# Kernel tuning notes

Hardware: AMD Instinct MI355X
Metric: run time of the kernel (lower is better)

The kernel has to match this reference:

```python
import jax, jax.numpy as jnp
import numpy as np

RADIUS = 1.3
RES = 128
SH_DEG = 2
N_SH = (SH_DEG + 1) ** 2          # 9 SH basis functions
DATA_DIM = N_SH * 3 + 1           # 28: 27 SH rgb coeffs + 1 sigma
STEP = (2.0 * RADIUS / RES) / 2.0 # half a voxel, as in calc_step_size
N_INTRS = int(np.ceil(np.sqrt(3.0) * 2.0 * RES))  # torch.arange(float) length
N_RAYS = 4096


def sh_basis(d):
    # Real spherical harmonics up to degree 2, svox2/plenoxels convention. d: [B,3]
    x, y, z = d[:, 0], d[:, 1], d[:, 2]
    return jnp.stack([
        0.28209479177387814 * jnp.ones_like(x),
        -0.4886025119029199 * y,
        0.4886025119029199 * z,
        -0.4886025119029199 * x,
        1.0925484305920792 * x * y,
        -1.0925484305920792 * y * z,
        0.31539156525252005 * (2.0 * z * z - x * x - y * y),
        -1.0925484305920792 * x * z,
        0.5462742152960396 * (x * x - y * y),
    ], axis=-1)  # [B, 9]


def trilerp(grid, pts):
    # grid: [C, R, R, R] laid out (D,H,W); pts: [N,3] as (x,y,z) in [-1,1],
    # x indexes W, y indexes H, z indexes D (torch grid_sample convention),
    # align_corners=True, padding_mode='border'. Returns [C, N].
    R = grid.shape[-1]
    c = jnp.clip((pts + 1.0) * 0.5 * (R - 1), 0.0, R - 1)  # border padding
    c0 = jnp.floor(c)
    f = c - c0
    i0 = c0.astype(jnp.int32)
    i1 = jnp.minimum(i0 + 1, R - 1)
    x0, y0, z0 = i0[:, 0], i0[:, 1], i0[:, 2]
    x1, y1, z1 = i1[:, 0], i1[:, 1], i1[:, 2]
    fx, fy, fz = f[:, 0], f[:, 1], f[:, 2]
    g = lambda zi, yi, xi: grid[:, zi, yi, xi]  # [C, N]
    out = (g(z0, y0, x0) * ((1 - fz) * (1 - fy) * (1 - fx)) +
           g(z0, y0, x1) * ((1 - fz) * (1 - fy) * fx) +
           g(z0, y1, x0) * ((1 - fz) * fy * (1 - fx)) +
           g(z0, y1, x1) * ((1 - fz) * fy * fx) +
           g(z1, y0, x0) * (fz * (1 - fy) * (1 - fx)) +
           g(z1, y0, x1) * (fz * (1 - fy) * fx) +
           g(z1, y1, x0) * (fz * fy * (1 - fx)) +
           g(z1, y1, x1) * (fz * fy * fx))
    return out


def setup_inputs() -> dict:
    key = jax.random.key(0)
    k1, k2, k3 = jax.random.split(key, 3)
    rays_o = jax.random.normal(k1, (N_RAYS, 3), jnp.float32) * 0.3  # inside cube
    rd = jax.random.normal(k2, (N_RAYS, 3), jnp.float32)
    rays_d = rd / jnp.linalg.norm(rd, axis=-1, keepdims=True)
    # grid parameter: SH coeffs init 0.1, sigma init 0.01 (as in module) + noise
    base = jnp.concatenate([
        jnp.full((1, DATA_DIM - 1, RES, RES, RES), 0.1, jnp.float32),
        jnp.full((1, 1, RES, RES, RES), 0.01, jnp.float32)], axis=1)
    data = base + 0.01 * jax.random.normal(k3, (1, DATA_DIM, RES, RES, RES), jnp.float32)
    return {"rays_o": rays_o, "rays_d": rays_d, "data": data}


def reference(rays_o, rays_d, data):
    # --- ray/box intersection sampling (no grad in original) ---
    ro = jax.lax.stop_gradient(rays_o)
    rd = jax.lax.stop_gradient(rays_d)
    off_pos = (RADIUS - ro) / rd
    off_neg = (-RADIUS - ro) / rd
    start = jnp.max(jnp.minimum(off_pos, off_neg), axis=-1, keepdims=True)  # [B,1]
    steps = jnp.arange(N_INTRS, dtype=ro.dtype)[None, :]
    intersections = start + steps * STEP          # [B, N_INTRS]
    t = intersections[:, :-1]                     # [B, NI]
    pts = ro[:, None, :] + t[..., None] * rd[:, None, :]  # [B, NI, 3]
    mask = jnp.all((pts > -RADIUS) & (pts < RADIUS), axis=-1)  # [B, NI]
    ptsn = pts / RADIUS
    B, NI = t.shape

    # --- trilinear interpolation of grid at all sample points ---
    interp = trilerp(data[0], ptsn.reshape(-1, 3)).T  # [B*NI, 28]
    sigma = jax.nn.relu(interp[:, -1].reshape(B, NI))
    sigma = jnp.where(mask, sigma, 0.0)  # masked_scatter into zeros

    # --- sigma2alpha: standard volumetric compositing weights ---
    dists = (intersections[:, 1:] - intersections[:, :-1]) \
            * jnp.linalg.norm(rays_d, axis=-1, keepdims=True)  # [B, NI]
    alpha = 1.0 - jnp.exp(-sigma * dists)
    trans = jnp.cumprod(jnp.concatenate(
        [jnp.ones((B, 1), alpha.dtype), 1.0 - alpha + 1e-10], axis=1), axis=1)[:, :-1]
    abs_light = alpha * trans  # [B, NI]

    # --- SH -> rgb per sample ---
    sh_mult = sh_basis(rays_d)  # [B, 9]
    sh = interp[:, :-1].reshape(B, NI, 3, N_SH)
    rgb_pts = jnp.einsum('bk,bnck->bnc', sh_mult, sh)  # [B, NI, 3]
    rgb_pts = jnp.where(mask[..., None], rgb_pts, 0.0)  # masked_scatter

    # --- shrgb2rgb: sigmoid, composite, white background ---
    rgb = jnp.sum(abs_light[..., None] * jax.nn.sigmoid(rgb_pts), axis=1)  # [B,3]
    rgb = rgb + (1.0 - jnp.sum(abs_light, axis=1))[..., None]  # white bkgd
    return rgb
```

## Files before the change

kernel.cpp:

```cpp
#include <hip/hip_runtime.h>
#include <math.h>


typedef _Float16 h8 __attribute__((ext_vector_type(8)));

namespace {
constexpr float kRadius   = 1.3f;
constexpr int   kRes      = 128;
constexpr float kStep     = 2.0f * 1.3f / 128.0f / 2.0f;
constexpr int   kNI       = 443;
constexpr int   kNRays    = 4096;
constexpr int   kChStride = kRes * kRes * kRes;
constexpr int   kChunks   = 7;
constexpr int   kCh       = 28;
constexpr int   kVoxPad   = 32;
constexpr size_t kVoxBytes = (size_t)kChStride * kVoxPad * sizeof(_Float16);
}

__global__ __launch_bounds__(256)
void convert_grid(const float* __restrict__ grid, _Float16* __restrict__ vox)
{
    const int v = blockIdx.x * 256 + threadIdx.x;
    h8 o[4];
    #pragma unroll
    for (int c = 0; c < kCh; ++c)
        o[c >> 3][c & 7] = (_Float16)grid[c * kChStride + v];
    o[3][4] = o[3][5] = o[3][6] = o[3][7] = (_Float16)0.f;

    h8* dst = (h8*)(vox + (size_t)v * kVoxPad);
    dst[0] = o[0]; dst[1] = o[1]; dst[2] = o[2]; dst[3] = o[3];
}

__global__ __launch_bounds__(256)
void render_chunks(const float* __restrict__ rays_o,
                   const float* __restrict__ rays_d,
                   const _Float16* __restrict__ vox,
                   float* __restrict__ partials)
{
    const int lane  = threadIdx.x & 63;
    const int W     = blockIdx.x * 4 + (threadIdx.x >> 6);
    const int ray   = W / 7;
    const int chunk = W - ray * 7;

    const float ox = rays_o[3*ray+0], oy = rays_o[3*ray+1], oz = rays_o[3*ray+2];
    const float dx = rays_d[3*ray+0], dy = rays_d[3*ray+1], dz = rays_d[3*ray+2];

    const float sx = fminf(( kRadius - ox)/dx, (-kRadius - ox)/dx);
    const float sy = fminf(( kRadius - oy)/dy, (-kRadius - oy)/dy);
    const float sz = fminf(( kRadius - oz)/dz, (-kRadius - oz)/dz);
    const float start = fmaxf(sx, fmaxf(sy, sz));
    const float dnorm = sqrtf(dx*dx + dy*dy + dz*dz);
    const float dist  = kStep * dnorm;

    float shm[9];
    shm[0] =  0.28209479177387814f;
    shm[1] = -0.4886025119029199f * dy;
    shm[2] =  0.4886025119029199f * dz;
    shm[3] = -0.4886025119029199f * dx;
    shm[4] =  1.0925484305920792f * dx * dy;
    shm[5] = -1.0925484305920792f * dy * dz;
    shm[6] =  0.31539156525252005f * (2.0f*dz*dz - dx*dx - dy*dy);
    shm[7] = -1.0925484305920792f * dx * dz;
    shm[8] =  0.5462742152960396f * (dx*dx - dy*dy);

    const int k = chunk * 64 + lane;

    float alpha = 0.0f;
    float a     = 1.0f;
    float rp0 = 0.f, rp1 = 0.f, rp2 = 0.f;
    bool  inb = false;

    if (k < kNI) {
        const float t  = start + (float)k * kStep;
        const float px = ox + t*dx;
        const float py = oy + t*dy;
        const float pz = oz + t*dz;
        inb = (px > -kRadius) && (px < kRadius) &&
              (py > -kRadius) && (py < kRadius) &&
              (pz > -kRadius) && (pz < kRadius);

        float sig = 0.0f;
        if (inb) {
            const float cx = fminf(fmaxf((px*(1.0f/kRadius) + 1.0f)*0.5f*127.0f, 0.0f), 127.0f);
            const float cy = fminf(fmaxf((py*(1.0f/kRadius) + 1.0f)*0.5f*127.0f, 0.0f), 127.0f);
            const float cz = fminf(fmaxf((pz*(1.0f/kRadius) + 1.0f)*0.5f*127.0f, 0.0f), 127.0f);
            const float fx0 = floorf(cx), fy0 = floorf(cy), fz0 = floorf(cz);
            const float fx = cx - fx0, fy = cy - fy0, fz = cz - fz0;
            const int ix0 = (int)fx0, iy0 = (int)fy0, iz0 = (int)fz0;
            const int ix1 = min(ix0 + 1, 127);
            const int iy1 = min(iy0 + 1, 127);
            const int iz1 = min(iz0 + 1, 127);

            const float gx0 = 1.0f - fx, gy0 = 1.0f - fy, gz0 = 1.0f - fz;

            const int offs[8] = {
                iz0*(kRes*kRes) + iy0*kRes + ix0,
                iz0*(kRes*kRes) + iy0*kRes + ix1,
                iz0*(kRes*kRes) + iy1*kRes + ix0,
                iz0*(kRes*kRes) + iy1*kRes + ix1,
                iz1*(kRes*kRes) + iy0*kRes + ix0,
                iz1*(kRes*kRes) + iy0*kRes + ix1,
                iz1*(kRes*kRes) + iy1*kRes + ix0,
                iz1*(kRes*kRes) + iy1*kRes + ix1 };
            const float cw[8] = {
                gz0*gy0*gx0, gz0*gy0*fx, gz0*fy*gx0, gz0*fy*fx,
                fz *gy0*gx0, fz *gy0*fx, fz *fy*gx0, fz *fy*fx };

            #pragma unroll
            for (int cn = 0; cn < 8; ++cn) {
                const h8* vp = (const h8*)(vox + (size_t)offs[cn] * kVoxPad);
                const h8 q0 = vp[0], q1 = vp[1], q2 = vp[2], q3 = vp[3];

                float f[28];
                #pragma unroll
                for (int i = 0; i < 8; ++i) f[i]      = (float)q0[i];
                #pragma unroll
                for (int i = 0; i < 8; ++i) f[8 + i]  = (float)q1[i];
                #pragma unroll
                for (int i = 0; i < 8; ++i) f[16 + i] = (float)q2[i];
                #pragma unroll
                for (int i = 0; i < 4; ++i) f[24 + i] = (float)q3[i];

                float r = 0.f, g = 0.f, b = 0.f;
                #pragma unroll
                for (int j = 0; j < 9; ++j) {
                    r = fmaf(shm[j], f[j],      r);
                    g = fmaf(shm[j], f[9 + j],  g);
                    b = fmaf(shm[j], f[18 + j], b);
                }
                const float wc = cw[cn];
                rp0 = fmaf(wc, r, rp0);
                rp1 = fmaf(wc, g, rp1);
                rp2 = fmaf(wc, b, rp2);
                sig = fmaf(wc, f[27], sig);
            }
            sig = fmaxf(sig, 0.0f);
        }
        alpha = 1.0f - expf(-sig * dist);
        a     = 1.0f - alpha + 1e-10f;
    }

    float prod = a;
    #pragma unroll
    for (int off = 1; off < 64; off <<= 1) {
        const float y = __shfl_up(prod, off, 64);
        if (lane >= off) prod *= y;
    }
    float excl = __shfl_up(prod, 1, 64);
    if (lane == 0) excl = 1.0f;

    const float w = alpha * excl;

    float sR = 0.f, sG = 0.f, sB = 0.f;
    if (inb) {
        sR = w * (1.0f / (1.0f + expf(-rp0)));
        sG = w * (1.0f / (1.0f + expf(-rp1)));
        sB = w * (1.0f / (1.0f + expf(-rp2)));
    }
    float sL = w;

    const float P = __shfl(prod, 63, 64);

    #pragma unroll
    for (int off = 32; off > 0; off >>= 1) {
        sR += __shfl_down(sR, off, 64);
        sG += __shfl_down(sG, off, 64);
        sB += __shfl_down(sB, off, 64);
        sL += __shfl_down(sL, off, 64);
    }

    if (lane == 0) {
        float* p = partials + (size_t)(ray * 7 + chunk) * 5;
        p[0] = sR; p[1] = sG; p[2] = sB; p[3] = sL; p[4] = P;
    }
}

__global__ __launch_bounds__(256)
void combine_chunks(const float* __restrict__ partials, float* __restrict__ out)
{
    const int r = blockIdx.x * 256 + threadIdx.x;
    const float* p = partials + (size_t)r * (kChunks * 5);

    float carry = 1.0f, aR = 0.f, aG = 0.f, aB = 0.f, aL = 0.f;
    #pragma unroll
    for (int c = 0; c < kChunks; ++c) {
        aR = fmaf(carry, p[c*5 + 0], aR);
        aG = fmaf(carry, p[c*5 + 1], aG);
        aB = fmaf(carry, p[c*5 + 2], aB);
        aL = fmaf(carry, p[c*5 + 3], aL);
        carry *= p[c*5 + 4];
    }
    const float bg = 1.0f - aL;
    out[3*r + 0] = aR + bg;
    out[3*r + 1] = aG + bg;
    out[3*r + 2] = aB + bg;
}

#define TRI8(p) (w000*(p)[o000] + w001*(p)[o001] + w010*(p)[o010] + w011*(p)[o011] \
               + w100*(p)[o100] + w101*(p)[o101] + w110*(p)[o110] + w111*(p)[o111])

__global__ __launch_bounds__(256)
void plenoxel_render_direct(const float* __restrict__ rays_o,
                            const float* __restrict__ rays_d,
                            const float* __restrict__ grid,
                            float* __restrict__ out)
{
    const int lane = threadIdx.x & 63;
    const int ray  = blockIdx.x * 4 + (threadIdx.x >> 6);

    const float ox = rays_o[3*ray+0], oy = rays_o[3*ray+1], oz = rays_o[3*ray+2];
    const float dx = rays_d[3*ray+0], dy = rays_d[3*ray+1], dz = rays_d[3*ray+2];

    const float sx = fminf(( kRadius - ox)/dx, (-kRadius - ox)/dx);
    const float sy = fminf(( kRadius - oy)/dy, (-kRadius - oy)/dy);
    const float sz = fminf(( kRadius - oz)/dz, (-kRadius - oz)/dz);
    const float start = fmaxf(sx, fmaxf(sy, sz));
    const float dnorm = sqrtf(dx*dx + dy*dy + dz*dz);

    float shm[9];
    shm[0] =  0.28209479177387814f;
    shm[1] = -0.4886025119029199f * dy;
    shm[2] =  0.4886025119029199f * dz;
    shm[3] = -0.4886025119029199f * dx;
    shm[4] =  1.0925484305920792f * dx * dy;
    shm[5] = -1.0925484305920792f * dy * dz;
    shm[6] =  0.31539156525252005f * (2.0f*dz*dz - dx*dx - dy*dy);
    shm[7] = -1.0925484305920792f * dx * dz;
    shm[8] =  0.5462742152960396f * (dx*dx - dy*dy);

    float carry = 1.0f;
    float accR = 0.f, accG = 0.f, accB = 0.f, accL = 0.f;

    for (int chunk = 0; chunk < kChunks; ++chunk) {
        const int k = chunk * 64 + lane;
        float alpha = 0.0f, a = 1.0f;
        float rp0 = 0.f, rp1 = 0.f, rp2 = 0.f;
        bool inb = false;

        if (k < kNI) {
            const float t = start + (float)k * kStep;
            const float dist = kStep * dnorm;
            const float px = ox + t*dx, py = oy + t*dy, pz = oz + t*dz;
            inb = (px > -kRadius) && (px < kRadius) &&
                  (py > -kRadius) && (py < kRadius) &&
                  (pz > -kRadius) && (pz < kRadius);
            float sigma = 0.0f;
            if (inb) {
                const float cx = fminf(fmaxf((px*(1.0f/kRadius) + 1.0f)*0.5f*127.0f, 0.0f), 127.0f);
                const float cy = fminf(fmaxf((py*(1.0f/kRadius) + 1.0f)*0.5f*127.0f, 0.0f), 127.0f);
                const float cz = fminf(fmaxf((pz*(1.0f/kRadius) + 1.0f)*0.5f*127.0f, 0.0f), 127.0f);
                const float fx0 = floorf(cx), fy0 = floorf(cy), fz0 = floorf(cz);
                const float fx = cx - fx0, fy = cy - fy0, fz = cz - fz0;
                const int ix0 = (int)fx0, iy0 = (int)fy0, iz0 = (int)fz0;
                const int ix1 = min(ix0 + 1, 127);
                const int iy1 = min(iy0 + 1, 127);
                const int iz1 = min(iz0 + 1, 127);
                const float gx0 = 1.0f - fx, gy0 = 1.0f - fy, gz0 = 1.0f - fz;
                const float w000 = gz0*gy0*gx0, w001 = gz0*gy0*fx;
                const float w010 = gz0*fy *gx0, w011 = gz0*fy *fx;
                const float w100 = fz *gy0*gx0, w101 = fz *gy0*fx;
                const float w110 = fz *fy *gx0, w111 = fz *fy *fx;
                const int o000 = iz0*(kRes*kRes) + iy0*kRes + ix0;
                const int o001 = iz0*(kRes*kRes) + iy0*kRes + ix1;
                const int o010 = iz0*(kRes*kRes) + iy1*kRes + ix0;
                const int o011 = iz0*(kRes*kRes) + iy1*kRes + ix1;
                const int o100 = iz1*(kRes*kRes) + iy0*kRes + ix0;
                const int o101 = iz1*(kRes*kRes) + iy0*kRes + ix1;
                const int o110 = iz1*(kRes*kRes) + iy1*kRes + ix0;
                const int o111 = iz1*(kRes*kRes) + iy1*kRes + ix1;
                #pragma unroll
                for (int kk = 0; kk < 9; ++kk) {
                    rp0 = fmaf(shm[kk], TRI8(grid + (kk     ) * kChStride), rp0);
                    rp1 = fmaf(shm[kk], TRI8(grid + (kk +  9) * kChStride), rp1);
                    rp2 = fmaf(shm[kk], TRI8(grid + (kk + 18) * kChStride), rp2);
                }
                sigma = fmaxf(TRI8(grid + 27 * kChStride), 0.0f);
            }
            alpha = 1.0f - expf(-sigma * dist);
            a     = 1.0f - alpha + 1e-10f;
        }

        float prod = a;
        #pragma unroll
        for (int off = 1; off < 64; off <<= 1) {
            const float y = __shfl_up(prod, off, 64);
            if (lane >= off) prod *= y;
        }
        float excl = __shfl_up(prod, 1, 64);
        if (lane == 0) excl = 1.0f;
        const float trans = carry * excl;
        const float w = alpha * trans;
        if (inb) {
            accR = fmaf(w, 1.0f / (1.0f + expf(-rp0)), accR);
            accG = fmaf(w, 1.0f / (1.0f + expf(-rp1)), accG);
            accB = fmaf(w, 1.0f / (1.0f + expf(-rp2)), accB);
        }
        accL += w;
        carry *= __shfl(prod, 63, 64);
    }

    #pragma unroll
    for (int off = 32; off > 0; off >>= 1) {
        accR += __shfl_down(accR, off, 64);
        accG += __shfl_down(accG, off, 64);
        accB += __shfl_down(accB, off, 64);
        accL += __shfl_down(accL, off, 64);
    }

    if (lane == 0) {
        const float bg = 1.0f - accL;
        out[3*ray + 0] = accR + bg;
        out[3*ray + 1] = accG + bg;
        out[3*ray + 2] = accB + bg;
    }
}

extern "C" void kernel_launch(void* const* d_in, const int* in_sizes, int n_in,
                              void* d_out, int out_size, void* d_ws, size_t ws_size,
                              hipStream_t stream) {
    const float* rays_o = (const float*)d_in[0];
    const float* rays_d = (const float*)d_in[1];
    const float* data   = (const float*)d_in[2];
    float* out = (float*)d_out;

    const size_t partBytes = (size_t)kNRays * kChunks * 5 * sizeof(float);
    const size_t need = kVoxBytes + partBytes;

    if (ws_size >= need) {
        _Float16* vox = (_Float16*)d_ws;
        float* partials = (float*)((char*)d_ws + kVoxBytes);

        hipLaunchKernelGGL(convert_grid,
                           dim3(kChStride / 256), dim3(256), 0, stream,
                           data, vox);
        hipLaunchKernelGGL(render_chunks,
                           dim3(kNRays * kChunks / 4), dim3(256), 0, stream,
                           rays_o, rays_d, vox, partials);
        hipLaunchKernelGGL(combine_chunks,
                           dim3(kNRays / 256), dim3(256), 0, stream,
                           partials, out);
    } else {
        hipLaunchKernelGGL(plenoxel_render_direct,
                           dim3(kNRays / 4), dim3(256), 0, stream,
                           rays_o, rays_d, data, out);
    }
}
```

Before: 435.6 us.

## Process two 64-sample segments per wave and cut ray chunks to four

```diff
diff --git a/kernel.cpp b/kernel.cpp
--- a/kernel.cpp
+++ b/kernel.cpp
@@ -11,10 +11,11 @@
 constexpr int   kNI       = 443;
 constexpr int   kNRays    = 4096;
 constexpr int   kChStride = kRes * kRes * kRes;
-constexpr int   kChunks   = 7;
 constexpr int   kCh       = 28;
 constexpr int   kVoxPad   = 32;
 constexpr size_t kVoxBytes = (size_t)kChStride * kVoxPad * sizeof(_Float16);
+constexpr int   kChunks4  = 4;
+constexpr int   kChunks7  = 7;
 }
 
 __global__ __launch_bounds__(256)
@@ -24,14 +25,100 @@
     h8 o[4];
     #pragma unroll
     for (int c = 0; c < kCh; ++c)
-        o[c >> 3][c & 7] = (_Float16)grid[c * kChStride + v];
+        o[c >> 3][c & 7] = (_Float16)__builtin_nontemporal_load(grid + (size_t)c * kChStride + v);
     o[3][4] = o[3][5] = o[3][6] = o[3][7] = (_Float16)0.f;
 
     h8* dst = (h8*)(vox + (size_t)v * kVoxPad);
     dst[0] = o[0]; dst[1] = o[1]; dst[2] = o[2]; dst[3] = o[3];
 }
 
-__global__ __launch_bounds__(256)
+struct Sample {
+    float alpha;
+    float a;
+    float rp0, rp1, rp2;
+    bool  inb;
+};
+
+__device__ __forceinline__ Sample eval_sample(
+    int k, float start, float ox, float oy, float oz,
+    float dx, float dy, float dz, float dist,
+    const float* __restrict__ shm, const _Float16* __restrict__ vox)
+{
+    Sample s;
+    s.alpha = 0.f; s.a = 1.f; s.rp0 = s.rp1 = s.rp2 = 0.f; s.inb = false;
+    if (k >= kNI) return s;
+
+    const float t  = start + (float)k * kStep;
+    const float px = ox + t*dx;
+    const float py = oy + t*dy;
+    const float pz = oz + t*dz;
+    s.inb = (px > -kRadius) && (px < kRadius) &&
+            (py > -kRadius) && (py < kRadius) &&
+            (pz > -kRadius) && (pz < kRadius);
+
+    float sig = 0.0f;
+    if (s.inb) {
+        const float cx = fminf(fmaxf((px*(1.0f/kRadius) + 1.0f)*0.5f*127.0f, 0.0f), 127.0f);
+        const float cy = fminf(fmaxf((py*(1.0f/kRadius) + 1.0f)*0.5f*127.0f, 0.0f), 127.0f);
+        const float cz = fminf(fmaxf((pz*(1.0f/kRadius) + 1.0f)*0.5f*127.0f, 0.0f), 127.0f);
+        const float fx0 = floorf(cx), fy0 = floorf(cy), fz0 = floorf(cz);
+        const float fx = cx - fx0, fy = cy - fy0, fz = cz - fz0;
+        const int ix0 = (int)fx0, iy0 = (int)fy0, iz0 = (int)fz0;
+        const int ix1 = min(ix0 + 1, 127);
+        const int iy1 = min(iy0 + 1, 127);
+        const int iz1 = min(iz0 + 1, 127);
+
+        const float gx0 = 1.0f - fx, gy0 = 1.0f - fy, gz0 = 1.0f - fz;
+
+        const int offs[8] = {
+            iz0*(kRes*kRes) + iy0*kRes + ix0,
+            iz0*(kRes*kRes) + iy0*kRes + ix1,
+            iz0*(kRes*kRes) + iy1*kRes + ix0,
+            iz0*(kRes*kRes) + iy1*kRes + ix1,
+            iz1*(kRes*kRes) + iy0*kRes + ix0,
+            iz1*(kRes*kRes) + iy0*kRes + ix1,
+            iz1*(kRes*kRes) + iy1*kRes + ix0,
+            iz1*(kRes*kRes) + iy1*kRes + ix1 };
+        const float cw[8] = {
+            gz0*gy0*gx0, gz0*gy0*fx, gz0*fy*gx0, gz0*fy*fx,
+            fz *gy0*gx0, fz *gy0*fx, fz *fy*gx0, fz *fy*fx };
+
+        #pragma unroll
+        for (int cn = 0; cn < 8; ++cn) {
+            const h8* vp = (const h8*)(vox + (size_t)offs[cn] * kVoxPad);
+            const h8 q0 = vp[0], q1 = vp[1], q2 = vp[2], q3 = vp[3];
+
+            float f[28];
+            #pragma unroll
+            for (int i = 0; i < 8; ++i) f[i]      = (float)q0[i];
+            #pragma unroll
+            for (int i = 0; i < 8; ++i) f[8 + i]  = (float)q1[i];
+            #pragma unroll
+            for (int i = 0; i < 8; ++i) f[16 + i] = (float)q2[i];
+            #pragma unroll
+            for (int i = 0; i < 4; ++i) f[24 + i] = (float)q3[i];
+
+            float r = 0.f, g = 0.f, b = 0.f;
+            #pragma unroll
+            for (int j = 0; j < 9; ++j) {
+                r = fmaf(shm[j], f[j],      r);
+                g = fmaf(shm[j], f[9 + j],  g);
+                b = fmaf(shm[j], f[18 + j], b);
+            }
+            const float wc = cw[cn];
+            s.rp0 = fmaf(wc, r, s.rp0);
+            s.rp1 = fmaf(wc, g, s.rp1);
+            s.rp2 = fmaf(wc, b, s.rp2);
+            sig   = fmaf(wc, f[27], sig);
+        }
+        sig = fmaxf(sig, 0.0f);
+    }
+    s.alpha = 1.0f - expf(-sig * dist);
+    s.a     = 1.0f - s.alpha + 1e-10f;
+    return s;
+}
+
+__global__ __launch_bounds__(256, 3)
 void render_chunks(const float* __restrict__ rays_o,
                    const float* __restrict__ rays_d,
                    const _Float16* __restrict__ vox,
@@ -39,8 +126,8 @@
 {
     const int lane  = threadIdx.x & 63;
     const int W     = blockIdx.x * 4 + (threadIdx.x >> 6);
-    const int ray   = W / 7;
-    const int chunk = W - ray * 7;
+    const int ray   = W >> 2;
+    const int chunk = W & 3;
 
     const float ox = rays_o[3*ray+0], oy = rays_o[3*ray+1], oz = rays_o[3*ray+2];
     const float dx = rays_d[3*ray+0], dy = rays_d[3*ray+1], dz = rays_d[3*ray+2];
@@ -63,103 +150,46 @@
     shm[7] = -1.0925484305920792f * dx * dz;
     shm[8] =  0.5462742152960396f * (dx*dx - dy*dy);
 
-    const int k = chunk * 64 + lane;
-
-    float alpha = 0.0f;
-    float a     = 1.0f;
-    float rp0 = 0.f, rp1 = 0.f, rp2 = 0.f;
-    bool  inb = false;
-
-    if (k < kNI) {
-        const float t  = start + (float)k * kStep;
-        const float px = ox + t*dx;
-        const float py = oy + t*dy;
-        const float pz = oz + t*dz;
-        inb = (px > -kRadius) && (px < kRadius) &&
-              (py > -kRadius) && (py < kRadius) &&
-              (pz > -kRadius) && (pz < kRadius);
-
-        float sig = 0.0f;
-        if (inb) {
-            const float cx = fminf(fmaxf((px*(1.0f/kRadius) + 1.0f)*0.5f*127.0f, 0.0f), 127.0f);
-            const float cy = fminf(fmaxf((py*(1.0f/kRadius) + 1.0f)*0.5f*127.0f, 0.0f), 127.0f);
-            const float cz = fminf(fmaxf((pz*(1.0f/kRadius) + 1.0f)*0.5f*127.0f, 0.0f), 127.0f);
-            const float fx0 = floorf(cx), fy0 = floorf(cy), fz0 = floorf(cz);
-            const float fx = cx - fx0, fy = cy - fy0, fz = cz - fz0;
-            const int ix0 = (int)fx0, iy0 = (int)fy0, iz0 = (int)fz0;
-            const int ix1 = min(ix0 + 1, 127);
-            const int iy1 = min(iy0 + 1, 127);
-            const int iz1 = min(iz0 + 1, 127);
-
-            const float gx0 = 1.0f - fx, gy0 = 1.0f - fy, gz0 = 1.0f - fz;
-
-            const int offs[8] = {
-                iz0*(kRes*kRes) + iy0*kRes + ix0,
-                iz0*(kRes*kRes) + iy0*kRes + ix1,
-                iz0*(kRes*kRes) + iy1*kRes + ix0,
-                iz0*(kRes*kRes) + iy1*kRes + ix1,
-                iz1*(kRes*kRes) + iy0*kRes + ix0,
-                iz1*(kRes*kRes) + iy0*kRes + ix1,
-                iz1*(kRes*kRes) + iy1*kRes + ix0,
-                iz1*(kRes*kRes) + iy1*kRes + ix1 };
-            const float cw[8] = {
-                gz0*gy0*gx0, gz0*gy0*fx, gz0*fy*gx0, gz0*fy*fx,
-                fz *gy0*gx0, fz *gy0*fx, fz *fy*gx0, fz *fy*fx };
-
-            #pragma unroll
-            for (int cn = 0; cn < 8; ++cn) {
-                const h8* vp = (const h8*)(vox + (size_t)offs[cn] * kVoxPad);
-                const h8 q0 = vp[0], q1 = vp[1], q2 = vp[2], q3 = vp[3];
-
-                float f[28];
-                #pragma unroll
-                for (int i = 0; i < 8; ++i) f[i]      = (float)q0[i];
-                #pragma unroll
-                for (int i = 0; i < 8; ++i) f[8 + i]  = (float)q1[i];
-                #pragma unroll
-                for (int i = 0; i < 8; ++i) f[16 + i] = (float)q2[i];
-                #pragma unroll
-                for (int i = 0; i < 4; ++i) f[24 + i] = (float)q3[i];
-
-                float r = 0.f, g = 0.f, b = 0.f;
-                #pragma unroll
-                for (int j = 0; j < 9; ++j) {
-                    r = fmaf(shm[j], f[j],      r);
-                    g = fmaf(shm[j], f[9 + j],  g);
-                    b = fmaf(shm[j], f[18 + j], b);
-                }
-                const float wc = cw[cn];
-                rp0 = fmaf(wc, r, rp0);
-                rp1 = fmaf(wc, g, rp1);
-                rp2 = fmaf(wc, b, rp2);
-                sig = fmaf(wc, f[27], sig);
-            }
-            sig = fmaxf(sig, 0.0f);
-        }
-        alpha = 1.0f - expf(-sig * dist);
-        a     = 1.0f - alpha + 1e-10f;
-    }
-
-    float prod = a;
+    const int base = chunk * 128;
+    const Sample A = eval_sample(base + lane,      start, ox, oy, oz, dx, dy, dz, dist, shm, vox);
+    const Sample B = eval_sample(base + 64 + lane, start, ox, oy, oz, dx, dy, dz, dist, shm, vox);
+
+    float prodA = A.a;
     #pragma unroll
     for (int off = 1; off < 64; off <<= 1) {
-        const float y = __shfl_up(prod, off, 64);
-        if (lane >= off) prod *= y;
-    }
-    float excl = __shfl_up(prod, 1, 64);
-    if (lane == 0) excl = 1.0f;
-
-    const float w = alpha * excl;
+        const float y = __shfl_up(prodA, off, 64);
+        if (lane >= off) prodA *= y;
+    }
+    float exclA = __shfl_up(prodA, 1, 64);
+    if (lane == 0) exclA = 1.0f;
+    const float P0 = __shfl(prodA, 63, 64);
+
+    float prodB = B.a;
+    #pragma unroll
+    for (int off = 1; off < 64; off <<= 1) {
+        const float y = __shfl_up(prodB, off, 64);
+        if (lane >= off) prodB *= y;
+    }
+    float exclB = __shfl_up(prodB, 1, 64);
+    if (lane == 0) exclB = 1.0f;
+    const float P1 = __shfl(prodB, 63, 64);
+
+    const float wA = A.alpha * exclA;
+    const float wB = B.alpha * P0 * exclB;
 
     float sR = 0.f, sG = 0.f, sB = 0.f;
-    if (inb) {
-        sR = w * (1.0f / (1.0f + expf(-rp0)));
-        sG = w * (1.0f / (1.0f + expf(-rp1)));
-        sB = w * (1.0f / (1.0f + expf(-rp2)));
-    }
-    float sL = w;
-
-    const float P = __shfl(prod, 63, 64);
+    if (A.inb) {
+        sR = wA * (1.0f / (1.0f + expf(-A.rp0)));
+        sG = wA * (1.0f / (1.0f + expf(-A.rp1)));
+        sB = wA * (1.0f / (1.0f + expf(-A.rp2)));
+    }
+    if (B.inb) {
+        sR = fmaf(wB, 1.0f / (1.0f + expf(-B.rp0)), sR);
+        sG = fmaf(wB, 1.0f / (1.0f + expf(-B.rp1)), sG);
+        sB = fmaf(wB, 1.0f / (1.0f + expf(-B.rp2)), sB);
+    }
+    float sL = wA + wB;
+    const float P = P0 * P1;
 
     #pragma unroll
     for (int off = 32; off > 0; off >>= 1) {
@@ -170,7 +200,7 @@
     }
 
     if (lane == 0) {
-        float* p = partials + (size_t)(ray * 7 + chunk) * 5;
+        float* p = partials + (size_t)(ray * kChunks4 + chunk) * 5;
         p[0] = sR; p[1] = sG; p[2] = sB; p[3] = sL; p[4] = P;
     }
 }
@@ -179,11 +209,11 @@
 void combine_chunks(const float* __restrict__ partials, float* __restrict__ out)
 {
     const int r = blockIdx.x * 256 + threadIdx.x;
-    const float* p = partials + (size_t)r * (kChunks * 5);
+    const float* p = partials + (size_t)r * (kChunks4 * 5);
 
     float carry = 1.0f, aR = 0.f, aG = 0.f, aB = 0.f, aL = 0.f;
     #pragma unroll
-    for (int c = 0; c < kChunks; ++c) {
+    for (int c = 0; c < kChunks4; ++c) {
         aR = fmaf(carry, p[c*5 + 0], aR);
         aG = fmaf(carry, p[c*5 + 1], aG);
         aB = fmaf(carry, p[c*5 + 2], aB);
@@ -231,7 +261,7 @@
     float carry = 1.0f;
     float accR = 0.f, accG = 0.f, accB = 0.f, accL = 0.f;
 
-    for (int chunk = 0; chunk < kChunks; ++chunk) {
+    for (int chunk = 0; chunk < kChunks7; ++chunk) {
         const int k = chunk * 64 + lane;
         float alpha = 0.0f, a = 1.0f;
         float rp0 = 0.f, rp1 = 0.f, rp2 = 0.f;
@@ -323,7 +353,7 @@
     const float* data   = (const float*)d_in[2];
     float* out = (float*)d_out;
 
-    const size_t partBytes = (size_t)kNRays * kChunks * 5 * sizeof(float);
+    const size_t partBytes = (size_t)kNRays * kChunks4 * 5 * sizeof(float);
     const size_t need = kVoxBytes + partBytes;
 
     if (ws_size >= need) {
@@ -334,7 +364,7 @@
                            dim3(kChStride / 256), dim3(256), 0, stream,
                            data, vox);
         hipLaunchKernelGGL(render_chunks,
-                           dim3(kNRays * kChunks / 4), dim3(256), 0, stream,
+                           dim3(kNRays * kChunks4 / 4), dim3(256), 0, stream,
                            rays_o, rays_d, vox, partials);
         hipLaunchKernelGGL(combine_chunks,
                            dim3(kNRays / 256), dim3(256), 0, stream,
```

New measurement: 403.6 us. 1.08x faster.
